# Performance work log

Measured on AMD Instinct MI355X. Metric: run time of the kernel, lower is better.

## Reference

```python
import jax, jax.numpy as jnp
import numpy as np

B, V, E = 1024, 50257, 128

def setup_inputs() -> dict:
    key = jax.random.key(0)
    k1, k2, k3, k4 = jax.random.split(key, 4)
    # xs: one-hot focus-word vectors [B, V]
    focus_ids = jax.random.randint(k1, (B,), 0, V)
    xs = jnp.zeros((B, V), dtype=jnp.float32).at[jnp.arange(B), focus_ids].set(1.0)
    metric = jax.random.normal(k2, (E, E), dtype=jnp.float32)
    EMBEDM = jax.random.normal(k3, (V, E), dtype=jnp.float32)
    NEGEMBEDM = jax.random.normal(k4, (V, E), dtype=jnp.float32)
    return {"xs": xs, "metric": metric, "EMBEDM": EMBEDM, "NEGEMBEDM": NEGEMBEDM}

def reference(xs, metric, EMBEDM, NEGEMBEDM):
    # xs @ EMBEDM : one-hot matmul == row gather, but kept as GEMM to match original math
    xsembeds = xs @ EMBEDM                              # [B, E]
    # dots(vs, ws, metric) = (vs @ metric) @ ws.T
    scores = (xsembeds @ metric) @ NEGEMBEDM.T          # [B, V]
    return jax.nn.log_softmax(scores, axis=1)
```

## Files before the change

### kernel.cpp

```cpp
#include <hip/hip_runtime.h>
#include <hip/hip_bf16.h>
#include <math.h>

#define B_ROWS 1024
#define V_COLS 50257
#define E_DIM  128
#define NTILES 393
#define VPAD   (NTILES * 128)
#define TPB    3
#define NX     131
#define N4     (V_COLS * E_DIM / 4)
#define N4P    (VPAD * E_DIM / 4)

typedef __attribute__((ext_vector_type(8))) short short8;
typedef __attribute__((ext_vector_type(4))) float floatx4;

static __device__ __forceinline__ unsigned short f2bf(float x) {
    union { float f; unsigned int u; } c; c.f = x;
    unsigned int u = c.u;
    unsigned int r = u + 0x7fffu + ((u >> 16) & 1u);
    return (unsigned short)(r >> 16);
}

__global__ void find_idx_kernel(const float4* __restrict__ xs4, int* __restrict__ idx) {
    long i = (long)blockIdx.x * blockDim.x + threadIdx.x;
    const long n4 = (long)B_ROWS * V_COLS / 4;
    if (i >= n4) return;
    float4 v = xs4[i];
    float vals[4] = {v.x, v.y, v.z, v.w};
    #pragma unroll
    for (int c = 0; c < 4; ++c) {
        if (vals[c] != 0.0f) {
            long f = 4 * i + c;
            int b = (int)(f / V_COLS);
            idx[b] = (int)(f - (long)b * V_COLS);
        }
    }
}

__global__ void cvt_bf16_kernel(const float4* __restrict__ src, ushort4* __restrict__ dst) {
    int i = blockIdx.x * blockDim.x + threadIdx.x;
    if (i >= N4P) return;
    ushort4 o;
    if (i < N4) {
        float4 v = src[i];
        o.x = f2bf(v.x); o.y = f2bf(v.y); o.z = f2bf(v.z); o.w = f2bf(v.w);
    } else {
        o.x = 0; o.y = 0; o.z = 0; o.w = 0;
    }
    dst[i] = o;
}

__global__ void compute_t_kernel(const float* __restrict__ EMB, const float* __restrict__ metric,
                                 const int* __restrict__ idx, unsigned short* __restrict__ t) {
    __shared__ float erow[E_DIM];
    int b = blockIdx.x, tid = threadIdx.x;
    int id = idx[b];
    erow[tid] = EMB[(long)id * E_DIM + tid];
    __syncthreads();
    float acc = 0.f;
    #pragma unroll 16
    for (int k = 0; k < E_DIM; ++k) acc += erow[k] * metric[k * E_DIM + tid];
    t[b * E_DIM + tid] = f2bf(acc);
}

template <bool WRITE_OUT>
__global__ __launch_bounds__(256, 2) void gemm_kernel(const unsigned short* __restrict__ t,
                                                      const unsigned short* __restrict__ neg,
                                                      float2* __restrict__ partials,
                                                      const float* __restrict__ lse,
                                                      float* __restrict__ out) {
    __shared__ float2 stats[2][128];

    const int tid  = threadIdx.x;
    const int lane = tid & 63, wave = tid >> 6;
    const int l16  = lane & 15, q = lane >> 4;
    const int wm   = wave >> 1, wn = wave & 1;
    const int mbase = blockIdx.x * 128;
    const int tile0 = blockIdx.y * TPB;

    short8 af[4][4];
    #pragma unroll
    for (int mf = 0; mf < 4; ++mf) {
        const unsigned short* arow = t + (size_t)(mbase + wm * 64 + mf * 16 + l16) * E_DIM + q * 8;
        #pragma unroll
        for (int ks = 0; ks < 4; ++ks)
            af[mf][ks] = *(const short8*)(arow + ks * 32);
    }

    float lsev[4][4];
    float rm[4][4], rs[4][4];
    if (WRITE_OUT) {
        #pragma unroll
        for (int mf = 0; mf < 4; ++mf)
            #pragma unroll
            for (int r = 0; r < 4; ++r)
                lsev[mf][r] = lse[mbase + wm * 64 + mf * 16 + q * 4 + r];
    } else {
        #pragma unroll
        for (int mf = 0; mf < 4; ++mf)
            #pragma unroll
            for (int r = 0; r < 4; ++r) { rm[mf][r] = -1e30f; rs[mf][r] = 0.f; }
    }

    for (int it = 0; it < TPB; ++it) {
        const int colbase = (tile0 + it) * 128 + wn * 64;

        short8 bf[4][4];
        #pragma unroll
        for (int nt = 0; nt < 4; ++nt) {
            const unsigned short* brow = neg + (size_t)(colbase + nt * 16 + l16) * E_DIM + q * 8;
            #pragma unroll
            for (int ks = 0; ks < 4; ++ks)
                bf[nt][ks] = *(const short8*)(brow + ks * 32);
        }

        floatx4 acc[4][4];
        #pragma unroll
        for (int mf = 0; mf < 4; ++mf)
            #pragma unroll
            for (int nt = 0; nt < 4; ++nt) acc[mf][nt] = (floatx4){0, 0, 0, 0};

        #pragma unroll
        for (int ks = 0; ks < 4; ++ks)
            #pragma unroll
            for (int mf = 0; mf < 4; ++mf)
                #pragma unroll
                for (int nt = 0; nt < 4; ++nt)
                    acc[mf][nt] = __builtin_amdgcn_mfma_f32_16x16x32_bf16(af[mf][ks], bf[nt][ks], acc[mf][nt], 0, 0, 0);

        if (WRITE_OUT) {
            #pragma unroll
            for (int nt = 0; nt < 4; ++nt) {
                const int col = colbase + nt * 16 + l16;
                if (col < V_COLS) {
                    #pragma unroll
                    for (int mf = 0; mf < 4; ++mf) {
                        const size_t rb = (size_t)(mbase + wm * 64 + mf * 16 + q * 4) * V_COLS + col;
                        #pragma unroll
                        for (int r = 0; r < 4; ++r)
                            out[rb + (size_t)r * V_COLS] = acc[mf][nt][r] - lsev[mf][r];
                    }
                }
            }
        } else {
            bool ok[4];
            #pragma unroll
            for (int nt = 0; nt < 4; ++nt) ok[nt] = (colbase + nt * 16 + l16) < V_COLS;
            #pragma unroll
            for (int mf = 0; mf < 4; ++mf)
                #pragma unroll
                for (int r = 0; r < 4; ++r) {
                    float m = rm[mf][r], s = rs[mf][r];
                    #pragma unroll
                    for (int nt = 0; nt < 4; ++nt) {
                        float v = acc[mf][nt][r];
                        float mm = ok[nt] ? fmaxf(m, v) : m;
                        s = s * __expf(m - mm) + (ok[nt] ? __expf(v - mm) : 0.f);
                        m = mm;
                    }
                    rm[mf][r] = m; rs[mf][r] = s;
                }
        }
    }

    if (!WRITE_OUT) {
        #pragma unroll
        for (int mf = 0; mf < 4; ++mf)
            #pragma unroll
            for (int r = 0; r < 4; ++r) {
                float m = rm[mf][r], s = rs[mf][r];
                #pragma unroll
                for (int d = 1; d < 16; d <<= 1) {
                    float m2 = __shfl_xor(m, d, 16);
                    float s2 = __shfl_xor(s, d, 16);
                    float mm = fmaxf(m, m2);
                    s = s * __expf(m - mm) + s2 * __expf(m2 - mm);
                    m = mm;
                }
                if (l16 == 0) stats[wn][wm * 64 + mf * 16 + q * 4 + r] = make_float2(m, s);
            }
        __syncthreads();
        if (tid < 128) {
            float2 p0 = stats[0][tid], p1 = stats[1][tid];
            float mm = fmaxf(p0.x, p1.x);
            float ss = p0.y * __expf(p0.x - mm) + p1.y * __expf(p1.x - mm);
            partials[(long)(mbase + tid) * NX + blockIdx.y] = make_float2(mm, ss);
        }
    }
}

__global__ void merge_lse_kernel(const float2* __restrict__ partials, float* __restrict__ lse) {
    int b = blockIdx.x;
    int tid = threadIdx.x;
    float m = -1e30f, s = 0.f;
    for (int i = tid; i < NX; i += 256) {
        float2 p = partials[(long)b * NX + i];
        float mm = fmaxf(m, p.x);
        s = s * __expf(m - mm) + p.y * __expf(p.x - mm);
        m = mm;
    }
    __shared__ float sm[256], ss[256];
    sm[tid] = m; ss[tid] = s;
    __syncthreads();
    for (int off = 128; off > 0; off >>= 1) {
        if (tid < off) {
            float m1 = sm[tid], s1 = ss[tid];
            float m2 = sm[tid + off], s2 = ss[tid + off];
            float mm = fmaxf(m1, m2);
            sm[tid] = mm;
            ss[tid] = s1 * __expf(m1 - mm) + s2 * __expf(m2 - mm);
        }
        __syncthreads();
    }
    if (tid == 0) lse[b] = sm[0] + __logf(ss[0]);
}

extern "C" void kernel_launch(void* const* d_in, const int* in_sizes, int n_in,
                              void* d_out, int out_size, void* d_ws, size_t ws_size,
                              hipStream_t stream) {
    const float* xs     = (const float*)d_in[0];
    const float* metric = (const float*)d_in[1];
    const float* EMB    = (const float*)d_in[2];
    const float* NEG    = (const float*)d_in[3];
    float* out = (float*)d_out;

    char* ws = (char*)d_ws;
    int*            idx      = (int*)ws;
    unsigned short* t        = (unsigned short*)(ws + 4096);
    unsigned short* neg16    = (unsigned short*)(ws + 266240);
    float2*         partials = (float2*)(ws + 13144064);
    float*          lse      = (float*)(ws + 14217216);

    {
        long n4 = (long)B_ROWS * V_COLS / 4;
        int blocks = (int)((n4 + 255) / 256);
        find_idx_kernel<<<blocks, 256, 0, stream>>>((const float4*)xs, idx);
    }
    cvt_bf16_kernel<<<(N4P + 255) / 256, 256, 0, stream>>>((const float4*)NEG, (ushort4*)neg16);
    compute_t_kernel<<<B_ROWS, E_DIM, 0, stream>>>(EMB, metric, idx, t);
    gemm_kernel<false><<<dim3(8, NX), 256, 0, stream>>>(t, neg16, partials, nullptr, nullptr);
    merge_lse_kernel<<<B_ROWS, 256, 0, stream>>>(partials, lse);
    gemm_kernel<true><<<dim3(8, NX), 256, 0, stream>>>(t, neg16, partials, lse, out);
}
```

Before: 511.1 us.

## Stage B tiles via direct-to-LDS loads and coalesce output stores through LDS

Each 128-column tile of NEGEMBEDM is now loaded once per block into a swizzled LDS buffer with global_load_lds. Waves then read their MFMA B fragments from LDS instead of issuing strided global loads per wave. In the output pass, accumulators are staged through a padded LDS tile so each row is written as contiguous 128-column runs rather than 16-float fragments. The online-softmax stats pass now does a per-tile max-then-sum and drops the per-column bounds mask, which assumes the padded columns past V do not distort the sum. The cost is added block barriers and extra LDS use that may lower occupancy.

```diff
diff --git a/kernel.cpp b/kernel.cpp
--- a/kernel.cpp
+++ b/kernel.cpp
@@ -14,6 +14,10 @@
 
 typedef __attribute__((ext_vector_type(8))) short short8;
 typedef __attribute__((ext_vector_type(4))) float floatx4;
+
+#define GLOAD_LDS16(g, l) \
+    __builtin_amdgcn_global_load_lds((const __attribute__((address_space(1))) void*)(g), \
+                                     (__attribute__((address_space(3))) void*)(l), 16, 0, 0)
 
 static __device__ __forceinline__ unsigned short f2bf(float x) {
     union { float f; unsigned int u; } c; c.f = x;
@@ -70,7 +74,10 @@
                                                       float2* __restrict__ partials,
                                                       const float* __restrict__ lse,
                                                       float* __restrict__ out) {
+    __shared__ __align__(16) uint4 Bbuf[2048];
+    __shared__ __align__(16) float sbuf[64 * 132];
     __shared__ float2 stats[2][128];
+    __shared__ float lsev[128];
 
     const int tid  = threadIdx.x;
     const int lane = tid & 63, wave = tid >> 6;
@@ -79,6 +86,8 @@
     const int mbase = blockIdx.x * 128;
     const int tile0 = blockIdx.y * TPB;
 
+    if (WRITE_OUT && tid < 128) lsev[tid] = lse[mbase + tid];
+
     short8 af[4][4];
     #pragma unroll
     for (int mf = 0; mf < 4; ++mf) {
@@ -88,79 +97,90 @@
             af[mf][ks] = *(const short8*)(arow + ks * 32);
     }
 
-    float lsev[4][4];
     float rm[4][4], rs[4][4];
-    if (WRITE_OUT) {
+    if (!WRITE_OUT) {
         #pragma unroll
         for (int mf = 0; mf < 4; ++mf)
             #pragma unroll
-            for (int r = 0; r < 4; ++r)
-                lsev[mf][r] = lse[mbase + wm * 64 + mf * 16 + q * 4 + r];
-    } else {
+            for (int r = 0; r < 4; ++r) { rm[mf][r] = -1e30f; rs[mf][r] = 0.f; }
+    }
+
+    for (int it = 0; it < TPB; ++it) {
+        const int tcol = (tile0 + it) * 128;
+
+        {
+            const char* gbase = (const char*)(neg + (size_t)tcol * E_DIM);
+            char* lbase = (char*)Bbuf + (size_t)(tid & ~63) * 16;
+            int s = tid;
+            #pragma unroll
+            for (int j = 0; j < 8; ++j) {
+                int row = s >> 4, cc = s & 15;
+                int gc = cc ^ (row & 15);
+                GLOAD_LDS16(gbase + (size_t)row * 256 + (size_t)gc * 16,
+                            lbase + (size_t)j * 4096);
+                s += 256;
+            }
+        }
+        __syncthreads();
+
+        floatx4 acc[4][4];
         #pragma unroll
         for (int mf = 0; mf < 4; ++mf)
             #pragma unroll
-            for (int r = 0; r < 4; ++r) { rm[mf][r] = -1e30f; rs[mf][r] = 0.f; }
-    }
-
-    for (int it = 0; it < TPB; ++it) {
-        const int colbase = (tile0 + it) * 128 + wn * 64;
-
-        short8 bf[4][4];
-        #pragma unroll
-        for (int nt = 0; nt < 4; ++nt) {
-            const unsigned short* brow = neg + (size_t)(colbase + nt * 16 + l16) * E_DIM + q * 8;
-            #pragma unroll
-            for (int ks = 0; ks < 4; ++ks)
-                bf[nt][ks] = *(const short8*)(brow + ks * 32);
-        }
-
-        floatx4 acc[4][4];
-        #pragma unroll
-        for (int mf = 0; mf < 4; ++mf)
-            #pragma unroll
             for (int nt = 0; nt < 4; ++nt) acc[mf][nt] = (floatx4){0, 0, 0, 0};
 
         #pragma unroll
-        for (int ks = 0; ks < 4; ++ks)
+        for (int ks = 0; ks < 4; ++ks) {
+            short8 bf[4];
+            #pragma unroll
+            for (int nt = 0; nt < 4; ++nt) {
+                int r = wn * 64 + nt * 16 + l16;
+                bf[nt] = *(const short8*)&Bbuf[r * 16 + ((ks * 4 + q) ^ (r & 15))];
+            }
             #pragma unroll
             for (int mf = 0; mf < 4; ++mf)
                 #pragma unroll
                 for (int nt = 0; nt < 4; ++nt)
-                    acc[mf][nt] = __builtin_amdgcn_mfma_f32_16x16x32_bf16(af[mf][ks], bf[nt][ks], acc[mf][nt], 0, 0, 0);
-
-        if (WRITE_OUT) {
-            #pragma unroll
-            for (int nt = 0; nt < 4; ++nt) {
-                const int col = colbase + nt * 16 + l16;
-                if (col < V_COLS) {
-                    #pragma unroll
-                    for (int mf = 0; mf < 4; ++mf) {
-                        const size_t rb = (size_t)(mbase + wm * 64 + mf * 16 + q * 4) * V_COLS + col;
-                        #pragma unroll
-                        for (int r = 0; r < 4; ++r)
-                            out[rb + (size_t)r * V_COLS] = acc[mf][nt][r] - lsev[mf][r];
-                    }
-                }
-            }
-        } else {
-            bool ok[4];
-            #pragma unroll
-            for (int nt = 0; nt < 4; ++nt) ok[nt] = (colbase + nt * 16 + l16) < V_COLS;
+                    acc[mf][nt] = __builtin_amdgcn_mfma_f32_16x16x32_bf16(af[mf][ks], bf[nt], acc[mf][nt], 0, 0, 0);
+        }
+        __syncthreads();
+
+        if (!WRITE_OUT) {
             #pragma unroll
             for (int mf = 0; mf < 4; ++mf)
                 #pragma unroll
                 for (int r = 0; r < 4; ++r) {
-                    float m = rm[mf][r], s = rs[mf][r];
+                    float a0 = acc[mf][0][r], a1 = acc[mf][1][r];
+                    float a2 = acc[mf][2][r], a3 = acc[mf][3][r];
+                    float tm = fmaxf(fmaxf(a0, a1), fmaxf(a2, a3));
+                    float ts = __expf(a0 - tm) + __expf(a1 - tm) + __expf(a2 - tm) + __expf(a3 - tm);
+                    float m = fmaxf(rm[mf][r], tm);
+                    rs[mf][r] = rs[mf][r] * __expf(rm[mf][r] - m) + ts * __expf(tm - m);
+                    rm[mf][r] = m;
+                }
+        } else {
+            #pragma unroll
+            for (int chunk = 0; chunk < 2; ++chunk) {
+                if (wm == chunk) {
                     #pragma unroll
-                    for (int nt = 0; nt < 4; ++nt) {
-                        float v = acc[mf][nt][r];
-                        float mm = ok[nt] ? fmaxf(m, v) : m;
-                        s = s * __expf(m - mm) + (ok[nt] ? __expf(v - mm) : 0.f);
-                        m = mm;
-                    }
-                    rm[mf][r] = m; rs[mf][r] = s;
-                }
+                    for (int mf = 0; mf < 4; ++mf)
+                        #pragma unroll
+                        for (int nt = 0; nt < 4; ++nt)
+                            #pragma unroll
+                            for (int r = 0; r < 4; ++r)
+                                sbuf[(mf * 16 + q * 4 + r) * 132 + wn * 64 + nt * 16 + l16] = acc[mf][nt][r];
+                }
+                __syncthreads();
+                #pragma unroll 4
+                for (int j = 0; j < 32; ++j) {
+                    int i = j * 256 + tid;
+                    int r = i >> 7, c = i & 127;
+                    int col = tcol + c;
+                    if (col < V_COLS)
+                        out[(size_t)(mbase + chunk * 64 + r) * V_COLS + col] = sbuf[r * 132 + c] - lsev[chunk * 64 + r];
+                }
+                __syncthreads();
+            }
         }
     }
 
```

After: 469.3 us. 8.2% less time.
